# Kernel optimization log

Measured on AMD Instinct MI355X. Metric: run time of the kernel, lower is better.

The kernel has to match this reference:

```python
import jax, jax.numpy as jnp
import numpy as np

FEATURE_DIM = 128
EDGE_DIM = 32
N_NODES = 10000
BATCH = 4
N_EDGES = 640000
TEMPERATURE = 0.66
POWER_ITERS = 5


def spectral_normalize(W):
    # torch.nn.utils.spectral_norm: divide W by largest singular value estimated
    # via power iteration; u, v are treated as constants (no grad).
    # W: [out, in]
    u = jnp.ones((W.shape[0],), W.dtype) / jnp.sqrt(jnp.asarray(W.shape[0], W.dtype))
    for _ in range(POWER_ITERS):
        v = W.T @ u
        v = v / (jnp.linalg.norm(v) + 1e-12)
        u = W @ v
        u = u / (jnp.linalg.norm(u) + 1e-12)
    u = jax.lax.stop_gradient(u)
    v = jax.lax.stop_gradient(v)
    sigma = u @ (W @ v)
    return W / sigma


def setup_inputs() -> dict:
    key = jax.random.key(0)
    ks = jax.random.split(key, 8)
    node_feat = jax.random.normal(ks[0], (BATCH, N_NODES, FEATURE_DIM), dtype=jnp.float32)
    batch_ids = jax.random.randint(ks[1], (N_EDGES,), 0, BATCH)
    src_nodes = jax.random.randint(ks[2], (N_EDGES,), 0, N_NODES)
    tgt_nodes = jax.random.randint(ks[3], (N_EDGES,), 0, N_NODES)
    in_dim = 2 * FEATURE_DIM + 1  # src_feat ++ tgt_feat ++ distance
    # kaiming_normal_(nonlinearity='relu'): std = sqrt(2 / fan_in)
    W1 = jax.random.normal(ks[4], (EDGE_DIM, in_dim), jnp.float32) * np.sqrt(2.0 / in_dim)
    b1 = jnp.zeros((EDGE_DIM,), jnp.float32)
    W2 = jax.random.normal(ks[5], (EDGE_DIM, EDGE_DIM), jnp.float32) * np.sqrt(2.0 / EDGE_DIM)
    b2 = jnp.zeros((EDGE_DIM,), jnp.float32)
    bound = 0.1 * np.sqrt(6.0 / (EDGE_DIM + 1))
    W3 = jax.random.uniform(ks[6], (1, EDGE_DIM), jnp.float32, -bound, bound)
    b3 = jnp.ones((1,), jnp.float32)
    return {"node_feat": node_feat, "W1": W1, "b1": b1, "W2": W2, "b2": b2,
            "W3": W3, "b3": b3, "batch_ids": batch_ids,
            "src_nodes": src_nodes, "tgt_nodes": tgt_nodes}


def reference(node_feat, W1, b1, W2, b2, W3, b3, batch_ids, src_nodes, tgt_nodes):
    # per-edge gather of endpoint features  [E, D]
    src_feat = node_feat[batch_ids, src_nodes]
    tgt_feat = node_feat[batch_ids, tgt_nodes]
    dist = jnp.linalg.norm(src_feat - tgt_feat, axis=-1, keepdims=True)  # [E,1]
    edge_features = jnp.concatenate([src_feat, tgt_feat, dist], axis=-1)  # [E, 2D+1]
    # spectral-norm MLP (dropout is identity at eval / in this reference)
    h = jax.nn.relu(edge_features @ spectral_normalize(W1).T + b1)
    h = jax.nn.relu(h @ spectral_normalize(W2).T + b2)
    logAlpha = (h @ spectral_normalize(W3).T + b3).squeeze(-1)  # [E]
    logAlpha = jnp.clip(logAlpha, -5.0, 5.0)
    edge_weights = jax.nn.sigmoid(logAlpha / TEMPERATURE)
    return edge_weights, logAlpha
```

## Files before the change

### kernel.cpp

```cpp
#include <hip/hip_runtime.h>
#include <hip/hip_fp16.h>
#include <math.h>

#define FEATD 128
#define NNODES 10000
#define NBATCH 4
#define NROWS (NBATCH*NNODES)

#define OFF_I1   0
#define OFF_W1L  8
#define OFF_W2   64
#define OFF_W3   1088
#define OFF_W2H  1120
#define OFF_P16  2048
#define P16_FLOATS (NROWS*64/2)
#define OFF_F16  (OFF_P16 + P16_FLOATS)
#define F16_FLOATS (NROWS*FEATD/2)
#define OFF_FBWT OFF_P16

typedef _Float16 h2 __attribute__((ext_vector_type(2)));
union U32H2 { unsigned u; h2 h; };
union U4H2  { uint4 u; h2 h[4]; };

#if defined(__has_builtin)
#if __has_builtin(__builtin_amdgcn_fdot2)
#define HAVE_FDOT2 1
#endif
#endif

__device__ __forceinline__ float fdot2f(h2 a, h2 b, float c) {
#ifdef HAVE_FDOT2
  return __builtin_amdgcn_fdot2(a, b, c, false);
#else
  return c + (float)a[0] * (float)b[0] + (float)a[1] * (float)b[1];
#endif
}

template <int M, int K>
__device__ float spectral_sigma_t(const float* __restrict__ Wg,
                                  float* sW, float* u, float* v, volatile float* red) {
  int tid = threadIdx.x;
  int wid = tid >> 6, lid = tid & 63;
  int j8 = tid >> 3, l8 = tid & 7;
  for (int i = tid; i < M * K; i += 256) sW[i] = Wg[i];
  if (tid < M) u[tid] = 1.0f;
  __syncthreads();
  float invu = 1.0f / sqrtf((float)M);
  float invv = 0.f;

  for (int it = 0; it < 5; ++it) {
    float p = 0.f;
    for (int k = tid; k < K; k += 256) {
      float a = 0.f;
      #pragma unroll
      for (int j = 0; j < M; ++j) a += sW[j * K + k] * u[j];
      a *= invu;
      v[k] = a;
      p += a * a;
    }
    #pragma unroll
    for (int off = 1; off < 64; off <<= 1) p += __shfl_xor(p, off, 64);
    if (lid == 0) red[wid] = p;
    __syncthreads();
    p = red[0] + red[1] + red[2] + red[3];
    invv = 1.0f / (sqrtf(p) + 1e-12f);

    float a = 0.f;
    if (j8 < M) {
      #pragma unroll
      for (int k = l8; k < K; k += 8) a += sW[j8 * K + k] * v[k];
      a *= invv;
    }
    a += __shfl_xor(a, 1, 64);
    a += __shfl_xor(a, 2, 64);
    a += __shfl_xor(a, 4, 64);
    float q = 0.f;
    if (j8 < M && l8 == 0) { u[j8] = a; q = a * a; }
    #pragma unroll
    for (int off = 1; off < 64; off <<= 1) q += __shfl_xor(q, off, 64);
    if (lid == 0) red[4 + wid] = q;
    __syncthreads();
    q = red[4] + red[5] + red[6] + red[7];
    invu = 1.0f / (sqrtf(q) + 1e-12f);
  }

  float a = 0.f;
  if (j8 < M) {
    #pragma unroll
    for (int k = l8; k < K; k += 8) a += sW[j8 * K + k] * v[k];
  }
  a += __shfl_xor(a, 1, 64);
  a += __shfl_xor(a, 2, 64);
  a += __shfl_xor(a, 4, 64);
  float s = (j8 < M && l8 == 0) ? a * u[j8] : 0.f;
  #pragma unroll
  for (int off = 1; off < 64; off <<= 1) s += __shfl_xor(s, off, 64);
  if (lid == 0) red[wid] = s;
  __syncthreads();
  float sig = (red[0] + red[1] + red[2] + red[3]) * invu * invv;
  __syncthreads();
  return sig;
}

__global__ __launch_bounds__(256) void prep_kernel(const float* __restrict__ feat,
                                                   const float* __restrict__ W1,
                                                   const float* __restrict__ W2,
                                                   const float* __restrict__ W3,
                                                   float* __restrict__ ws,
                                                   int doF16) {
  __shared__ float sA[32 * 257];
  __shared__ float u[32], v[257];
  __shared__ float red[8];
  int tid = threadIdx.x;

  if (blockIdx.x == 0) {
    float sig1 = spectral_sigma_t<32, 257>(W1, sA, u, v, red);
    float i1 = 1.0f / sig1;
    if (tid == 0) ws[OFF_I1] = i1;
    for (int j = tid; j < 32; j += 256) ws[OFF_W1L + j] = sA[j * 257 + 256] * i1;
    __syncthreads();
    float sig2 = spectral_sigma_t<32, 32>(W2, sA, u, v, red);
    float i2 = 1.0f / sig2;
    for (int idx = tid; idx < 1024; idx += 256) ws[OFF_W2 + idx] = sA[idx] * i2;
    unsigned* w2h = (unsigned*)(ws + OFF_W2H);
    for (int idx = tid; idx < 512; idx += 256) {
      int j = idx >> 4, q = idx & 15;
      U32H2 pk;
      pk.h[0] = (_Float16)(sA[j * 32 + 2 * q] * i2);
      pk.h[1] = (_Float16)(sA[j * 32 + 2 * q + 1] * i2);
      w2h[idx] = pk.u;
    }
    __syncthreads();
    float sig3 = spectral_sigma_t<1, 32>(W3, sA, u, v, red);
    float i3 = 1.0f / sig3;
    for (int k = tid; k < 32; k += 256) ws[OFF_W3 + k] = sA[k] * i3;
    return;
  }

  for (int idx = tid; idx < 32 * 257; idx += 256) {
    int j = idx / 257, c = idx - j * 257;
    float w = W1[idx];
    if (c < 128) sA[c * 64 + j] = w;
    else if (c < 256) sA[(c - 128) * 64 + 32 + j] = w;
  }
  __syncthreads();

  __half* p16 = (__half*)(ws + OFF_P16);
  __half* f16 = (__half*)(ws + OFF_F16);
  int nl = tid >> 3;
  int jg = (tid & 7) << 3;
  int slice = (tid & 7);
  int c = blockIdx.x - 1;
  int r0 = c * 64 + nl * 2;
  int r1 = r0 + 1;
  const float4* F0 = (const float4*)&feat[(size_t)r0 * FEATD];
  const float4* F1 = (const float4*)&feat[(size_t)r1 * FEATD];
  float acc0[8] = {0,0,0,0,0,0,0,0};
  float acc1[8] = {0,0,0,0,0,0,0,0};
  #pragma unroll 2
  for (int k4 = 0; k4 < 32; ++k4) {
    float4 f0 = F0[k4];
    float4 f1 = F1[k4];
    if (doF16 && (k4 >> 2) == slice) {
      U32H2 a, b;
      uint2 pk;
      a.h[0] = (_Float16)f0.x; a.h[1] = (_Float16)f0.y; pk.x = a.u;
      b.h[0] = (_Float16)f0.z; b.h[1] = (_Float16)f0.w; pk.y = b.u;
      *(uint2*)((char*)f16 + (size_t)r0 * 256 + (size_t)k4 * 8) = pk;
      a.h[0] = (_Float16)f1.x; a.h[1] = (_Float16)f1.y; pk.x = a.u;
      b.h[0] = (_Float16)f1.z; b.h[1] = (_Float16)f1.w; pk.y = b.u;
      *(uint2*)((char*)f16 + (size_t)r1 * 256 + (size_t)k4 * 8) = pk;
    }
    #pragma unroll
    for (int kk = 0; kk < 4; ++kk) {
      int k = 4 * k4 + kk;
      float fv0 = (kk == 0) ? f0.x : (kk == 1) ? f0.y : (kk == 2) ? f0.z : f0.w;
      float fv1 = (kk == 0) ? f1.x : (kk == 1) ? f1.y : (kk == 2) ? f1.z : f1.w;
      float4 w0 = *(const float4*)&sA[k * 64 + jg];
      float4 w1 = *(const float4*)&sA[k * 64 + jg + 4];
      acc0[0] += fv0 * w0.x; acc0[1] += fv0 * w0.y; acc0[2] += fv0 * w0.z; acc0[3] += fv0 * w0.w;
      acc0[4] += fv0 * w1.x; acc0[5] += fv0 * w1.y; acc0[6] += fv0 * w1.z; acc0[7] += fv0 * w1.w;
      acc1[0] += fv1 * w0.x; acc1[1] += fv1 * w0.y; acc1[2] += fv1 * w0.z; acc1[3] += fv1 * w0.w;
      acc1[4] += fv1 * w1.x; acc1[5] += fv1 * w1.y; acc1[6] += fv1 * w1.z; acc1[7] += fv1 * w1.w;
    }
  }
  U32H2 t0, t1, t2, t3;
  uint4 o;
  t0.h[0]=(_Float16)acc0[0]; t0.h[1]=(_Float16)acc0[1];
  t1.h[0]=(_Float16)acc0[2]; t1.h[1]=(_Float16)acc0[3];
  t2.h[0]=(_Float16)acc0[4]; t2.h[1]=(_Float16)acc0[5];
  t3.h[0]=(_Float16)acc0[6]; t3.h[1]=(_Float16)acc0[7];
  o.x=t0.u; o.y=t1.u; o.z=t2.u; o.w=t3.u;
  *(uint4*)((char*)p16 + (size_t)r0 * 128 + (size_t)jg * 2) = o;
  t0.h[0]=(_Float16)acc1[0]; t0.h[1]=(_Float16)acc1[1];
  t1.h[0]=(_Float16)acc1[2]; t1.h[1]=(_Float16)acc1[3];
  t2.h[0]=(_Float16)acc1[4]; t2.h[1]=(_Float16)acc1[5];
  t3.h[0]=(_Float16)acc1[6]; t3.h[1]=(_Float16)acc1[7];
  o.x=t0.u; o.y=t1.u; o.z=t2.u; o.w=t3.u;
  *(uint4*)((char*)p16 + (size_t)r1 * 128 + (size_t)jg * 2) = o;
}

__device__ __forceinline__ float grp_dist_f16(uint4 au, uint4 bu) {
  U4H2 a, b; a.u = au; b.u = bu;
  float ssd = 0.f;
  #pragma unroll
  for (int p = 0; p < 4; ++p) { h2 d = a.h[p] - b.h[p]; ssd = fdot2f(d, d, ssd); }
  ssd += __shfl_xor(ssd, 1, 64);
  ssd += __shfl_xor(ssd, 2, 64);
  ssd += __shfl_xor(ssd, 4, 64);
  ssd += __shfl_xor(ssd, 8, 64);
  return sqrtf(ssd);
}

__device__ __forceinline__ unsigned h1pack(unsigned puv, unsigned quv, float dist, float i1,
                                           float w1l0, float w1l1, float bb0, float bb1) {
  U32H2 p, q; p.u = puv; q.u = quv;
  float h0  = fmaxf(fmaf((float)p.h[0] + (float)q.h[0], i1, fmaf(dist, w1l0, bb0)), 0.f);
  float h1v = fmaxf(fmaf((float)p.h[1] + (float)q.h[1], i1, fmaf(dist, w1l1, bb1)), 0.f);
  U32H2 r; r.h[0] = (_Float16)h0; r.h[1] = (_Float16)h1v;
  return r.u;
}

template <bool F16>
__global__ __launch_bounds__(256, 8) void edge_fused(const float* __restrict__ feat,
                                                     const float* __restrict__ ws,
                                                     const float* __restrict__ b1,
                                                     const float* __restrict__ b2,
                                                     const float* __restrict__ b3,
                                                     const int* __restrict__ bids,
                                                     const int* __restrict__ srcs,
                                                     const int* __restrict__ tgts,
                                                     float* __restrict__ out, int E) {
  __shared__ unsigned ht[256 * 17];
  __shared__ int sRS[256], sRT[256];
  int tid = threadIdx.x;
  int lane = tid & 15;
  int grp  = tid >> 4;

  const __half* feat16 = (const __half*)(ws + OFF_F16);
  const __half* p16    = (const __half*)(ws + OFF_P16);
  const unsigned* w2h  = (const unsigned*)(ws + OFF_W2H);

  float i1 = ws[OFF_I1];
  int j0 = 2 * lane;
  float w1l0 = ws[OFF_W1L + j0];
  float w1l1 = ws[OFF_W1L + j0 + 1];
  float bb0  = b1[j0];
  float bb1  = b1[j0 + 1];
  float bias3 = b3[0];

  for (int base = blockIdx.x * 256; base < E; base += gridDim.x * 256) {
    int e0 = base + tid;
    if (e0 < E) {
      int b = bids[e0];
      sRS[tid] = b * NNODES + srcs[e0];
      sRT[tid] = b * NNODES + tgts[e0];
    }
    __syncthreads();

    if (F16 && (base + 256 <= E)) {
      #pragma unroll 1
      for (int rr = 0; rr < 8; ++rr) {
        int el0 = (rr * 2 + 0) * 16 + grp;
        int el1 = (rr * 2 + 1) * 16 + grp;
        int rs0 = sRS[el0], rt0 = sRT[el0];
        int rs1 = sRS[el1], rt1 = sRT[el1];
        uint4 a0 = *(const uint4*)((const char*)feat16 + ((size_t)rs0 << 8) + (lane << 4));
        uint4 c0 = *(const uint4*)((const char*)feat16 + ((size_t)rt0 << 8) + (lane << 4));
        uint4 a1 = *(const uint4*)((const char*)feat16 + ((size_t)rs1 << 8) + (lane << 4));
        uint4 c1 = *(const uint4*)((const char*)feat16 + ((size_t)rt1 << 8) + (lane << 4));
        unsigned pu0 = *(const unsigned*)((const char*)p16 + ((size_t)rs0 << 7) + (lane << 2));
        unsigned qu0 = *(const unsigned*)((const char*)p16 + ((size_t)rt0 << 7) + 64 + (lane << 2));
        unsigned pu1 = *(const unsigned*)((const char*)p16 + ((size_t)rs1 << 7) + (lane << 2));
        unsigned qu1 = *(const unsigned*)((const char*)p16 + ((size_t)rt1 << 7) + 64 + (lane << 2));
        float d0 = grp_dist_f16(a0, c0);
        float d1 = grp_dist_f16(a1, c1);
        ht[el0 * 17 + lane] = h1pack(pu0, qu0, d0, i1, w1l0, w1l1, bb0, bb1);
        ht[el1 * 17 + lane] = h1pack(pu1, qu1, d1, i1, w1l0, w1l1, bb0, bb1);
      }
    } else {
      #pragma unroll 2
      for (int r = 0; r < 16; ++r) {
        int el = r * 16 + grp;
        int e  = base + el;
        if (e < E) {
          int rs = sRS[el], rt = sRT[el];
          float dist;
          if (F16) {
            uint4 au = *(const uint4*)((const char*)feat16 + ((size_t)rs << 8) + (lane << 4));
            uint4 bu = *(const uint4*)((const char*)feat16 + ((size_t)rt << 8) + (lane << 4));
            dist = grp_dist_f16(au, bu);
          } else {
            const float4* A  = (const float4*)&feat[(size_t)rs * FEATD];
            const float4* Bp = (const float4*)&feat[(size_t)rt * FEATD];
            float ssd = 0.f;
            #pragma unroll
            for (int p = 0; p < 2; ++p) {
              float4 a = A[lane * 2 + p], c = Bp[lane * 2 + p];
              float dx = a.x - c.x, dy = a.y - c.y, dz = a.z - c.z, dw = a.w - c.w;
              ssd += dx * dx + dy * dy + dz * dz + dw * dw;
            }
            ssd += __shfl_xor(ssd, 1, 64);
            ssd += __shfl_xor(ssd, 2, 64);
            ssd += __shfl_xor(ssd, 4, 64);
            ssd += __shfl_xor(ssd, 8, 64);
            dist = sqrtf(ssd);
          }
          unsigned puv = *(const unsigned*)((const char*)p16 + ((size_t)rs << 7) + (lane << 2));
          unsigned quv = *(const unsigned*)((const char*)p16 + ((size_t)rt << 7) + 64 + (lane << 2));
          ht[el * 17 + lane] = h1pack(puv, quv, dist, i1, w1l0, w1l1, bb0, bb1);
        }
      }
    }
    __syncthreads();

    int e = base + tid;
    if (e < E) {
      unsigned hrow[16];
      #pragma unroll
      for (int q = 0; q < 16; ++q) hrow[q] = ht[tid * 17 + q];
      float la = bias3;
      #pragma unroll
      for (int j = 0; j < 32; ++j) {
        float acc = b2[j];
        #pragma unroll
        for (int q = 0; q < 16; ++q) {
          U32H2 w; w.u = w2h[j * 16 + q];
          U32H2 h; h.u = hrow[q];
          acc = fdot2f(w.h, h.h, acc);
        }
        la += ws[OFF_W3 + j] * fmaxf(acc, 0.f);
      }
      la = fminf(fmaxf(la, -5.f), 5.f);
      out[e]     = 1.0f / (1.0f + exp2f(la * -2.18590179f));
      out[E + e] = la;
    }
    __syncthreads();
  }
}

__global__ __launch_bounds__(256) void spectral_full(const float* __restrict__ W1,
                                                     const float* __restrict__ W2,
                                                     const float* __restrict__ W3,
                                                     float* __restrict__ ws) {
  __shared__ float sA[32 * 257];
  __shared__ float u[32], v[257];
  __shared__ float red[8];
  int tid = threadIdx.x;
  float sig1 = spectral_sigma_t<32, 257>(W1, sA, u, v, red);
  float i1 = 1.0f / sig1;
  for (int idx = tid; idx < 128 * 64; idx += 256) {
    int k = idx >> 6, jj = idx & 63;
    float w = (jj < 32) ? sA[jj * 257 + k] : sA[(jj - 32) * 257 + 128 + k];
    ws[OFF_FBWT + idx] = w * i1;
  }
  for (int j = tid; j < 32; j += 256) ws[OFF_W1L + j] = sA[j * 257 + 256] * i1;
  __syncthreads();
  float sig2 = spectral_sigma_t<32, 32>(W2, sA, u, v, red);
  float i2 = 1.0f / sig2;
  for (int idx = tid; idx < 1024; idx += 256) ws[OFF_W2 + idx] = sA[idx] * i2;
  __syncthreads();
  float sig3 = spectral_sigma_t<1, 32>(W3, sA, u, v, red);
  float i3 = 1.0f / sig3;
  for (int k = tid; k < 32; k += 256) ws[OFF_W3 + k] = sA[k] * i3;
}

__global__ __launch_bounds__(256) void edge_kernel_nop(const float* __restrict__ feat,
                                                       const float* __restrict__ ws,
                                                       const float* __restrict__ b1,
                                                       const float* __restrict__ b2,
                                                       const float* __restrict__ b3,
                                                       const int* __restrict__ bids,
                                                       const int* __restrict__ srcs,
                                                       const int* __restrict__ tgts,
                                                       float* __restrict__ out, int E) {
  __shared__ float sWt[128 * 64];
  __shared__ float sW2[1024];
  __shared__ float sW3[32], sW1l[32], sB1[32], sB2[32];
  int tid = threadIdx.x;
  for (int i = tid * 4; i < 128 * 64; i += 256 * 4)
    *(float4*)&sWt[i] = *(const float4*)&ws[OFF_FBWT + i];
  for (int i = tid; i < 1024; i += 256) sW2[i] = ws[OFF_W2 + i];
  if (tid < 32) {
    sW3[tid]  = ws[OFF_W3 + tid];
    sW1l[tid] = ws[OFF_W1L + tid];
    sB1[tid]  = b1[tid];
    sB2[tid]  = b2[tid];
  }
  __syncthreads();
  float bias3 = b3[0];

  for (int e = blockIdx.x * 256 + tid; e < E; e += gridDim.x * 256) {
    int b = bids[e], s = srcs[e], t = tgts[e];
    const float4* A  = (const float4*)&feat[(size_t)(b * NNODES + s) * FEATD];
    const float4* Bp = (const float4*)&feat[(size_t)(b * NNODES + t) * FEATD];
    float ssd = 0.f;
    float h1p[32];
    #pragma unroll
    for (int j = 0; j < 32; ++j) h1p[j] = 0.f;
    #pragma unroll 1
    for (int k4 = 0; k4 < 32; ++k4) {
      float4 a = A[k4], c = Bp[k4];
      float dx = a.x - c.x, dy = a.y - c.y, dz = a.z - c.z, dw = a.w - c.w;
      ssd += dx * dx + dy * dy + dz * dz + dw * dw;
      #pragma unroll
      for (int kk = 0; kk < 4; ++kk) {
        int k = 4 * k4 + kk;
        float fa = (kk == 0) ? a.x : (kk == 1) ? a.y : (kk == 2) ? a.z : a.w;
        float fc = (kk == 0) ? c.x : (kk == 1) ? c.y : (kk == 2) ? c.z : c.w;
        #pragma unroll
        for (int q = 0; q < 8; ++q) {
          float4 w0 = *(const float4*)&sWt[k * 64 + 4 * q];
          float4 w1 = *(const float4*)&sWt[k * 64 + 32 + 4 * q];
          h1p[4*q+0] += fa * w0.x + fc * w1.x;
          h1p[4*q+1] += fa * w0.y + fc * w1.y;
          h1p[4*q+2] += fa * w0.z + fc * w1.z;
          h1p[4*q+3] += fa * w0.w + fc * w1.w;
        }
      }
    }
    float dist = sqrtf(ssd);
    float h1[32];
    #pragma unroll
    for (int j = 0; j < 32; ++j)
      h1[j] = fmaxf(h1p[j] + dist * sW1l[j] + sB1[j], 0.f);
    float la = bias3;
    #pragma unroll
    for (int j = 0; j < 32; ++j) {
      float acc = sB2[j];
      #pragma unroll
      for (int q = 0; q < 8; ++q) {
        float4 w = *(const float4*)&sW2[j * 32 + 4 * q];
        acc += w.x * h1[4 * q] + w.y * h1[4 * q + 1] + w.z * h1[4 * q + 2] + w.w * h1[4 * q + 3];
      }
      la += sW3[j] * fmaxf(acc, 0.f);
    }
    la = fminf(fmaxf(la, -5.f), 5.f);
    out[e]     = 1.0f / (1.0f + __expf(-la / 0.66f));
    out[E + e] = la;
  }
}

extern "C" void kernel_launch(void* const* d_in, const int* in_sizes, int n_in,
                              void* d_out, int out_size, void* d_ws, size_t ws_size,
                              hipStream_t stream) {
  const float* feat = (const float*)d_in[0];
  const float* W1   = (const float*)d_in[1];
  const float* b1   = (const float*)d_in[2];
  const float* W2   = (const float*)d_in[3];
  const float* b2   = (const float*)d_in[4];
  const float* W3   = (const float*)d_in[5];
  const float* b3   = (const float*)d_in[6];
  const int* bids   = (const int*)d_in[7];
  const int* srcs   = (const int*)d_in[8];
  const int* tgts   = (const int*)d_in[9];
  float* out = (float*)d_out;
  float* ws  = (float*)d_ws;
  int E = in_sizes[7];

  size_t need_p   = (size_t)OFF_F16 * sizeof(float);
  size_t need_f16 = (size_t)(OFF_F16 + F16_FLOATS) * sizeof(float);
  int egrid = (E + 255) / 256;

  if (ws_size >= need_f16) {
    prep_kernel<<<dim3(626), dim3(256), 0, stream>>>(feat, W1, W2, W3, ws, 1);
    edge_fused<true><<<dim3(egrid), dim3(256), 0, stream>>>(feat, ws, b1, b2, b3,
                                                            bids, srcs, tgts, out, E);
  } else if (ws_size >= need_p) {
    prep_kernel<<<dim3(626), dim3(256), 0, stream>>>(feat, W1, W2, W3, ws, 0);
    edge_fused<false><<<dim3(egrid), dim3(256), 0, stream>>>(feat, ws, b1, b2, b3,
                                                             bids, srcs, tgts, out, E);
  } else {
    spectral_full<<<dim3(1), dim3(256), 0, stream>>>(W1, W2, W3, ws);
    edge_kernel_nop<<<dim3(egrid), dim3(256), 0, stream>>>(feat, ws, b1, b2, b3,
                                                           bids, srcs, tgts, out, E);
  }
}
```

Baseline: 110.1 us.

## Bucket edges by batch and process each batch in a separate launch for L2 locality

Adds a counting sort (count, scan, scatter) that groups edges by batch id into a record buffer holding precomputed row indices and the original edge index. Four per-batch edge kernel launches then run over these segments, so that each launch gathers from only one batch's node tables, a working set small enough to stay in cache. The cost is three extra kernels, more launches, an extra write and read of 16-byte records per edge, and outputs that are now written in scattered order.

```diff
diff --git a/kernel.cpp b/kernel.cpp
--- a/kernel.cpp
+++ b/kernel.cpp
@@ -12,10 +12,14 @@
 #define OFF_W2   64
 #define OFF_W3   1088
 #define OFF_W2H  1120
-#define OFF_P16  2048
+#define OFF_SEG  1664
+#define OFF_BC   1680
+#define OFF_BASE 2704
+#define OFF_P16  4096
 #define P16_FLOATS (NROWS*64/2)
 #define OFF_F16  (OFF_P16 + P16_FLOATS)
 #define F16_FLOATS (NROWS*FEATD/2)
+#define OFF_REC  (OFF_F16 + F16_FLOATS)
 #define OFF_FBWT OFF_P16
 
 typedef _Float16 h2 __attribute__((ext_vector_type(2)));
@@ -200,6 +204,63 @@
   *(uint4*)((char*)p16 + (size_t)r1 * 128 + (size_t)jg * 2) = o;
 }
 
+__global__ __launch_bounds__(256) void bucket_count(const int* __restrict__ bids,
+                                                    int* __restrict__ wsI, int E) {
+  __shared__ int cnt[4];
+  int tid = threadIdx.x;
+  if (tid < 4) cnt[tid] = 0;
+  __syncthreads();
+  int chunk = (E + 255) / 256;
+  int cs = blockIdx.x * chunk;
+  int ce = min(cs + chunk, E);
+  for (int i = cs + tid; i < ce; i += 256) atomicAdd(&cnt[bids[i]], 1);
+  __syncthreads();
+  if (tid < 4) wsI[OFF_BC + blockIdx.x * 4 + tid] = cnt[tid];
+}
+
+__global__ __launch_bounds__(256) void bucket_scan(int* __restrict__ wsI, int E) {
+  __shared__ int A[1024], B[1024];
+  int tid = threadIdx.x;
+  for (int i = tid; i < 1024; i += 256) {
+    int blk = i & 255, b = i >> 8;
+    A[i] = wsI[OFF_BC + blk * 4 + b];
+  }
+  __syncthreads();
+  int* s = A; int* d = B;
+  for (int off = 1; off < 1024; off <<= 1) {
+    for (int i = tid; i < 1024; i += 256)
+      d[i] = s[i] + ((i >= off) ? s[i - off] : 0);
+    __syncthreads();
+    int* t = s; s = d; d = t;
+  }
+  for (int i = tid; i < 1024; i += 256) {
+    int excl = i ? s[i - 1] : 0;
+    int blk = i & 255, b = i >> 8;
+    wsI[OFF_BASE + blk * 4 + b] = excl;
+  }
+  if (tid < 4) wsI[OFF_SEG + tid] = tid ? s[tid * 256 - 1] : 0;
+  if (tid == 4) wsI[OFF_SEG + 4] = s[1023];
+}
+
+__global__ __launch_bounds__(256) void bucket_scatter(const int* __restrict__ bids,
+                                                      const int* __restrict__ srcs,
+                                                      const int* __restrict__ tgts,
+                                                      int* __restrict__ wsI, int E) {
+  __shared__ int cur[4];
+  int tid = threadIdx.x;
+  if (tid < 4) cur[tid] = wsI[OFF_BASE + blockIdx.x * 4 + tid];
+  __syncthreads();
+  int chunk = (E + 255) / 256;
+  int cs = blockIdx.x * chunk;
+  int ce = min(cs + chunk, E);
+  int4* rec = (int4*)(wsI + OFF_REC);
+  for (int i = cs + tid; i < ce; i += 256) {
+    int b = bids[i];
+    int pos = atomicAdd(&cur[b], 1);
+    rec[pos] = make_int4(b * NNODES + srcs[i], b * NNODES + tgts[i], i, 0);
+  }
+}
+
 __device__ __forceinline__ float grp_dist_f16(uint4 au, uint4 bu) {
   U4H2 a, b; a.u = au; b.u = bu;
   float ssd = 0.f;
@@ -219,6 +280,105 @@
   float h1v = fmaxf(fmaf((float)p.h[1] + (float)q.h[1], i1, fmaf(dist, w1l1, bb1)), 0.f);
   U32H2 r; r.h[0] = (_Float16)h0; r.h[1] = (_Float16)h1v;
   return r.u;
+}
+
+__global__ __launch_bounds__(256, 8) void edge_seg(const float* __restrict__ ws,
+                                                   const float* __restrict__ b1,
+                                                   const float* __restrict__ b2,
+                                                   const float* __restrict__ b3,
+                                                   float* __restrict__ out, int E, int bi) {
+  __shared__ unsigned ht[256 * 17];
+  __shared__ int sRS[256], sRT[256];
+  int tid = threadIdx.x;
+  int lane = tid & 15;
+  int grp  = tid >> 4;
+
+  const int* wsI = (const int*)ws;
+  const __half* feat16 = (const __half*)(ws + OFF_F16);
+  const __half* p16    = (const __half*)(ws + OFF_P16);
+  const unsigned* w2h  = (const unsigned*)(ws + OFF_W2H);
+  const int4* rec = (const int4*)(wsI + OFF_REC);
+
+  int start = wsI[OFF_SEG + bi];
+  int end   = wsI[OFF_SEG + bi + 1];
+
+  float i1 = ws[OFF_I1];
+  int j0 = 2 * lane;
+  float w1l0 = ws[OFF_W1L + j0];
+  float w1l1 = ws[OFF_W1L + j0 + 1];
+  float bb0  = b1[j0];
+  float bb1  = b1[j0 + 1];
+  float bias3 = b3[0];
+
+  for (int base = start + blockIdx.x * 256; base < end; base += gridDim.x * 256) {
+    int n = min(256, end - base);
+    int4 r = make_int4(0, 0, 0, 0);
+    if (tid < n) {
+      r = rec[base + tid];
+      sRS[tid] = r.x;
+      sRT[tid] = r.y;
+    }
+    __syncthreads();
+
+    if (n == 256) {
+      #pragma unroll 1
+      for (int rr = 0; rr < 8; ++rr) {
+        int el0 = (rr * 2 + 0) * 16 + grp;
+        int el1 = (rr * 2 + 1) * 16 + grp;
+        int rs0 = sRS[el0], rt0 = sRT[el0];
+        int rs1 = sRS[el1], rt1 = sRT[el1];
+        uint4 a0 = *(const uint4*)((const char*)feat16 + ((size_t)rs0 << 8) + (lane << 4));
+        uint4 c0 = *(const uint4*)((const char*)feat16 + ((size_t)rt0 << 8) + (lane << 4));
+        uint4 a1 = *(const uint4*)((const char*)feat16 + ((size_t)rs1 << 8) + (lane << 4));
+        uint4 c1 = *(const uint4*)((const char*)feat16 + ((size_t)rt1 << 8) + (lane << 4));
+        unsigned pu0 = *(const unsigned*)((const char*)p16 + ((size_t)rs0 << 7) + (lane << 2));
+        unsigned qu0 = *(const unsigned*)((const char*)p16 + ((size_t)rt0 << 7) + 64 + (lane << 2));
+        unsigned pu1 = *(const unsigned*)((const char*)p16 + ((size_t)rs1 << 7) + (lane << 2));
+        unsigned qu1 = *(const unsigned*)((const char*)p16 + ((size_t)rt1 << 7) + 64 + (lane << 2));
+        float d0 = grp_dist_f16(a0, c0);
+        float d1 = grp_dist_f16(a1, c1);
+        ht[el0 * 17 + lane] = h1pack(pu0, qu0, d0, i1, w1l0, w1l1, bb0, bb1);
+        ht[el1 * 17 + lane] = h1pack(pu1, qu1, d1, i1, w1l0, w1l1, bb0, bb1);
+      }
+    } else {
+      #pragma unroll 2
+      for (int rr = 0; rr < 16; ++rr) {
+        int el = rr * 16 + grp;
+        if (el < n) {
+          int rs = sRS[el], rt = sRT[el];
+          uint4 au = *(const uint4*)((const char*)feat16 + ((size_t)rs << 8) + (lane << 4));
+          uint4 bu = *(const uint4*)((const char*)feat16 + ((size_t)rt << 8) + (lane << 4));
+          float dist = grp_dist_f16(au, bu);
+          unsigned puv = *(const unsigned*)((const char*)p16 + ((size_t)rs << 7) + (lane << 2));
+          unsigned quv = *(const unsigned*)((const char*)p16 + ((size_t)rt << 7) + 64 + (lane << 2));
+          ht[el * 17 + lane] = h1pack(puv, quv, dist, i1, w1l0, w1l1, bb0, bb1);
+        }
+      }
+    }
+    __syncthreads();
+
+    if (tid < n) {
+      unsigned hrow[16];
+      #pragma unroll
+      for (int q = 0; q < 16; ++q) hrow[q] = ht[tid * 17 + q];
+      float la = bias3;
+      #pragma unroll
+      for (int j = 0; j < 32; ++j) {
+        float acc = b2[j];
+        #pragma unroll
+        for (int q = 0; q < 16; ++q) {
+          U32H2 w; w.u = w2h[j * 16 + q];
+          U32H2 h; h.u = hrow[q];
+          acc = fdot2f(w.h, h.h, acc);
+        }
+        la += ws[OFF_W3 + j] * fmaxf(acc, 0.f);
+      }
+      la = fminf(fmaxf(la, -5.f), 5.f);
+      out[r.z]     = 1.0f / (1.0f + exp2f(la * -2.18590179f));
+      out[E + r.z] = la;
+    }
+    __syncthreads();
+  }
 }
 
 template <bool F16>
@@ -280,8 +440,8 @@
       }
     } else {
       #pragma unroll 2
-      for (int r = 0; r < 16; ++r) {
-        int el = r * 16 + grp;
+      for (int rr = 0; rr < 16; ++rr) {
+        int el = rr * 16 + grp;
         int e  = base + el;
         if (e < E) {
           int rs = sRS[el], rt = sRT[el];
@@ -456,13 +616,23 @@
   const int* tgts   = (const int*)d_in[9];
   float* out = (float*)d_out;
   float* ws  = (float*)d_ws;
+  int* wsI   = (int*)d_ws;
   int E = in_sizes[7];
 
   size_t need_p   = (size_t)OFF_F16 * sizeof(float);
   size_t need_f16 = (size_t)(OFF_F16 + F16_FLOATS) * sizeof(float);
+  size_t need_rec = ((size_t)OFF_REC + (size_t)E * 4) * sizeof(float);
   int egrid = (E + 255) / 256;
 
-  if (ws_size >= need_f16) {
+  if (ws_size >= need_rec) {
+    prep_kernel<<<dim3(626), dim3(256), 0, stream>>>(feat, W1, W2, W3, ws, 1);
+    bucket_count<<<dim3(256), dim3(256), 0, stream>>>(bids, wsI, E);
+    bucket_scan<<<dim3(1), dim3(256), 0, stream>>>(wsI, E);
+    bucket_scatter<<<dim3(256), dim3(256), 0, stream>>>(bids, srcs, tgts, wsI, E);
+    int gseg = (E / 4 + 8192 + 255) / 256;
+    for (int bi = 0; bi < 4; ++bi)
+      edge_seg<<<dim3(gseg), dim3(256), 0, stream>>>(ws, b1, b2, b3, out, E, bi);
+  } else if (ws_size >= need_f16) {
     prep_kernel<<<dim3(626), dim3(256), 0, stream>>>(feat, W1, W2, W3, ws, 1);
     edge_fused<true><<<dim3(egrid), dim3(256), 0, stream>>>(feat, ws, b1, b2, b3,
                                                             bids, srcs, tgts, out, E);
```

Measured after the change: 154.8 us. 40.5% more time.
